# Kernel optimization log

Measured on AMD Instinct MI355X. Metric: run time of the kernel, lower is better.

## Reference

```python
import jax, jax.numpy as jnp
import numpy as np

D_MODEL = 1024
H = 16
D_K = D_MODEL // H
MASK_VALUE = -2000000000.0  # fp32 path in the original module


def setup_inputs() -> dict:
    key = jax.random.key(0)
    ks = jax.random.split(key, 7)
    B, S = 2, 2048
    scale = 1.0 / np.sqrt(D_MODEL)
    inp = {
        "q": jax.random.normal(ks[0], (B, S, D_MODEL), jnp.float32),
        "k": jax.random.normal(ks[1], (B, S, D_MODEL), jnp.float32),
        "v": jax.random.normal(ks[2], (B, S, D_MODEL), jnp.float32),
        # causal mask, broadcast over batch and heads
        "mask": jnp.tril(jnp.ones((1, 1, S, S), jnp.int32)),
        "w_q": jax.random.normal(ks[3], (D_MODEL, D_MODEL), jnp.float32) * scale,
        "w_k": jax.random.normal(ks[4], (D_MODEL, D_MODEL), jnp.float32) * scale,
        "w_v": jax.random.normal(ks[5], (D_MODEL, D_MODEL), jnp.float32) * scale,
        "w_o": jax.random.normal(ks[6], (D_MODEL, D_MODEL), jnp.float32) * scale,
    }
    return inp


def reference(q, k, v, mask, w_q, w_k, w_v, w_o):
    B, S, _ = q.shape
    # Linear(d_model, d_model, bias=False): x @ W.T  (weights stored [out, in])
    def proj(x, w):
        y = jnp.einsum('bsd,ed->bse', x, w)
        return y.reshape(B, -1, H, D_K).transpose(0, 2, 1, 3)  # [B, H, S, d_k]

    Q = proj(q, w_q)
    K = proj(k, w_k)
    V = proj(v, w_v)

    scores = jnp.einsum('bhsd,bhtd->bhst', Q, K) * (D_K ** -0.5)  # [B,H,S,S]
    scores = jnp.where(mask == 0, MASK_VALUE, scores)
    attn = jax.nn.softmax(scores, axis=-1)
    x = jnp.einsum('bhst,bhtd->bhsd', attn, V)                     # [B,H,S,d_k]
    x = x.transpose(0, 2, 1, 3).reshape(B, -1, D_MODEL)            # [B,S,d_model]
    return jnp.einsum('bsd,ed->bse', x, w_o)
```

## Files before the change

kernel.cpp:

```cpp
#include <hip/hip_runtime.h>
#include <math.h>

#define S_LEN 2048
#define DM 1024
#define NH 16
#define DK 64
#define BATCH 2
#define MS (BATCH*S_LEN)

typedef __attribute__((ext_vector_type(8))) short bf16x8;
typedef __attribute__((ext_vector_type(4))) float f32x4;
typedef __attribute__((ext_vector_type(16))) float f32x16;
typedef unsigned short u16;
typedef unsigned int u32;

__device__ __forceinline__ u16 f2b(float f) {
  union { float f; u32 u; } x; x.f = f;
  u32 r = x.u + 0x7FFFu + ((x.u >> 16) & 1u);
  return (u16)(r >> 16);
}

__device__ __forceinline__ u32 cvtpk_bf16(float lo, float hi) {
  u32 r;
  asm volatile("v_cvt_pk_bf16_f32 %0, %1, %2" : "=v"(r) : "v"(lo), "v"(hi));
  return r;
}

struct CvtArgs {
  const float* src[7];
  u16* dst[7];
  float scl[7];
  int n4[7];
};

__global__ void cvt_all(CvtArgs a) {
  const int seg = blockIdx.y;
  const float* __restrict__ in = a.src[seg];
  u16* __restrict__ out = a.dst[seg];
  const float s = a.scl[seg];
  const int n4 = a.n4[seg];
  int idx = blockIdx.x * blockDim.x + threadIdx.x;
  int stride = gridDim.x * blockDim.x;
  for (int i = idx; i < n4; i += stride) {
    float4 v = ((const float4*)in)[i];
    ushort4 o;
    o.x = f2b(v.x * s); o.y = f2b(v.y * s); o.z = f2b(v.z * s); o.w = f2b(v.w * s);
    ((ushort4*)out)[i] = o;
  }
}

__device__ __forceinline__ void gload_lds16(const u16* g, u16* l) {
  __builtin_amdgcn_global_load_lds((const __attribute__((address_space(1))) u32*)g,
                                   (__attribute__((address_space(3))) u32*)l, 16, 0, 0);
}

template<bool OUT_BF16, int BM>
__device__ __forceinline__ void gemm_body(
    const u16* __restrict__ A, const u16* __restrict__ B, void* __restrict__ Cout,
    int M, int N, int K, int bx, int by, u16* lsA, u16* lsB)
{
  constexpr int MF = BM / 32;
  const int tid = threadIdx.x;
  const int lane = tid & 63;
  const int wid = tid >> 6;
  const int wr = wid >> 1, wc = wid & 1;
  const int m0 = by * BM, n0 = bx * 128;

  f32x4 acc[MF][4];
#pragma unroll
  for (int i = 0; i < MF; ++i)
#pragma unroll
    for (int j = 0; j < 4; ++j) acc[i][j] = (f32x4){0.f, 0.f, 0.f, 0.f};

  const int ntiles = K >> 5;

#pragma unroll
  for (int i = 0; i < BM/64; ++i) {
    int u = tid + i * 256;
    gload_lds16(A + (size_t)(m0 + (u >> 2)) * K + (u & 3) * 8, &lsA[u * 8]);
  }
#pragma unroll
  for (int i = 0; i < 2; ++i) {
    int u = tid + i * 256;
    gload_lds16(B + (size_t)(n0 + (u >> 2)) * K + (u & 3) * 8, &lsB[u * 8]);
  }

  for (int kt = 0; kt < ntiles; ++kt) {
    __syncthreads();
    bf16x8 af[MF], bfr[4];
    const int kOff = (lane >> 4) * 8;
#pragma unroll
    for (int m = 0; m < MF; ++m)
      af[m] = *(const bf16x8*)&lsA[(wr * (BM/2) + m * 16 + (lane & 15)) * 32 + kOff];
#pragma unroll
    for (int n = 0; n < 4; ++n)
      bfr[n] = *(const bf16x8*)&lsB[(wc * 64 + n * 16 + (lane & 15)) * 32 + kOff];
    __syncthreads();
    if (kt + 1 < ntiles) {
      int k0 = (kt + 1) << 5;
#pragma unroll
      for (int i = 0; i < BM/64; ++i) {
        int u = tid + i * 256;
        gload_lds16(A + (size_t)(m0 + (u >> 2)) * K + k0 + (u & 3) * 8, &lsA[u * 8]);
      }
#pragma unroll
      for (int i = 0; i < 2; ++i) {
        int u = tid + i * 256;
        gload_lds16(B + (size_t)(n0 + (u >> 2)) * K + k0 + (u & 3) * 8, &lsB[u * 8]);
      }
    }
#pragma unroll
    for (int m = 0; m < MF; ++m)
#pragma unroll
      for (int n = 0; n < 4; ++n)
        acc[m][n] = __builtin_amdgcn_mfma_f32_16x16x32_bf16(af[m], bfr[n], acc[m][n], 0, 0, 0);
  }

  const int rbase = m0 + wr * (BM/2) + ((lane >> 4) << 2);
  const int cbase = n0 + wc * 64 + (lane & 15);
#pragma unroll
  for (int m = 0; m < MF; ++m)
#pragma unroll
    for (int n = 0; n < 4; ++n)
#pragma unroll
      for (int j = 0; j < 4; ++j) {
        int r = rbase + m * 16 + j;
        int c = cbase + n * 16;
        if (OUT_BF16)
          ((u16*)Cout)[(size_t)r * N + c] = f2b(acc[m][n][j]);
        else
          ((float*)Cout)[(size_t)r * N + c] = acc[m][n][j];
      }
}

struct G3Args {
  const u16* A[3];
  const u16* B[3];
  u16* C[3];
};

__global__ __launch_bounds__(256) void gemm_qkv(G3Args g) {
  __shared__ u16 lsA[128*32];
  __shared__ u16 lsB[128*32];
  const int bid = blockIdx.x;
  const int gi = bid >> 8;
  const int f = bid & 255;
  const int gx = (gi == 2) ? 32 : 8;
  const int N = (gi == 2) ? MS : DM;
  const int M = (gi == 2) ? DM : MS;
  gemm_body<true,128>(g.A[gi], g.B[gi], g.C[gi], M, N, DM,
                      f % gx, f / gx, lsA, lsB);
}

__global__ __launch_bounds__(256) void gemm_out(
    const u16* __restrict__ A, const u16* __restrict__ B, float* __restrict__ C) {
  __shared__ u16 lsA[64*32];
  __shared__ u16 lsB[128*32];
  gemm_body<false,64>(A, B, C, MS, DM, DM, blockIdx.x, blockIdx.y, lsA, lsB);
}

__global__ __launch_bounds__(256) void attn_fwd(
    const u16* __restrict__ Qp, const u16* __restrict__ Kp, const u16* __restrict__ Vt,
    u16* __restrict__ AO)
{
  __shared__ __align__(16) u16 lds_kv[4][4096];
  __shared__ float lds_l[4][2][32];
  const int tid = threadIdx.x;
  const int lane = tid & 63;
  const int w = tid >> 6;
  const int ql = lane & 31;
  const int h = lane >> 5;
  const int bid = blockIdx.x;
  const int j = 63 - (bid >> 5);
  const int bh = bid & 31;
  const int b = bh >> 4;
  const int hh = bh & 15;
  const int q0 = j * 32;
  const int qg = q0 + ql;
  const size_t baseQK = (size_t)b * S_LEN * DM + hh * DK;
  const size_t baseV  = (size_t)hh * DK * MS + (size_t)b * S_LEN;

  u16* const lk = lds_kv[w];
  u16* const lv = lds_kv[w] + 2048;

  bf16x8 qf[4];
#pragma unroll
  for (int ks = 0; ks < 4; ++ks)
    qf[ks] = *(const bf16x8*)&Qp[baseQK + (size_t)qg * DM + ks * 16 + h * 8];

  f32x16 ot[2];
#pragma unroll
  for (int n = 0; n < 2; ++n)
#pragma unroll
    for (int r = 0; r < 16; ++r) ot[n][r] = 0.f;
  float lrun = 0.f;

#define STAGE(KV0) do { \
    _Pragma("unroll") \
    for (int jj = 0; jj < 4; ++jj) { \
      int c = jj * 64 + lane; \
      int kr = c >> 3, kc = c & 7; \
      gload_lds16(Kp + baseQK + (size_t)((KV0) + kr) * DM + ((kc ^ (kr & 7)) * 8), &lk[c * 8]); \
      int vr = c >> 2, vc = c & 3; \
      gload_lds16(Vt + baseV + (size_t)vr * MS + (KV0) + ((vc ^ (vr & 3)) * 8), &lv[c * 8]); \
    } \
  } while (0)

  if (w <= j) STAGE(w * 32);

  for (int tt = w; tt <= j; tt += 4) {
    asm volatile("s_waitcnt vmcnt(0)" ::: "memory");

    bf16x8 kf[4], vf[2][2];
#pragma unroll
    for (int ks = 0; ks < 4; ++ks)
      kf[ks] = *(const bf16x8*)&lk[(ql * 8 + ((2 * ks + h) ^ (ql & 7))) * 8];
#pragma unroll
    for (int n = 0; n < 2; ++n)
#pragma unroll
      for (int kst = 0; kst < 2; ++kst)
        vf[n][kst] = *(const bf16x8*)&lv[((n * 32 + ql) * 4 + ((2 * kst + h) ^ (ql & 3))) * 8];
    asm volatile("s_waitcnt lgkmcnt(0)" ::: "memory");
    if (tt + 4 <= j) STAGE((tt + 4) * 32);

    f32x16 st;
#pragma unroll
    for (int r = 0; r < 16; ++r) st[r] = 0.f;
    __builtin_amdgcn_s_setprio(1);
#pragma unroll
    for (int ks = 0; ks < 4; ++ks)
      st = __builtin_amdgcn_mfma_f32_32x32x16_bf16(kf[ks], qf[ks], st, 0, 0, 0);
    __builtin_amdgcn_s_setprio(0);

    if (tt == j) {
#pragma unroll
      for (int r = 0; r < 16; ++r) {
        int kvg = tt * 32 + (r & 3) + 8 * (r >> 2) + 4 * h;
        if (kvg > qg) st[r] = -1e30f;
      }
    }

#pragma unroll
    for (int r = 0; r < 16; ++r) {
      float p_ = st[r];
      asm("v_exp_f32 %0, %1" : "=v"(p_) : "v"(p_));
      st[r] = p_;
    }
    {
      float t0 = st[0] + st[1], t1 = st[2] + st[3];
      float t2 = st[4] + st[5], t3 = st[6] + st[7];
      float t4 = st[8] + st[9], t5 = st[10] + st[11];
      float t6 = st[12] + st[13], t7 = st[14] + st[15];
      float u0 = t0 + t1, u1 = t2 + t3, u2 = t4 + t5, u3 = t6 + t7;
      lrun += (u0 + u1) + (u2 + u3);
    }

#pragma unroll
    for (int kst = 0; kst < 2; ++kst) {
      u32 pkg[4];
#pragma unroll
      for (int g4 = 0; g4 < 4; ++g4)
        pkg[g4] = cvtpk_bf16(st[8 * kst + 2 * g4], st[8 * kst + 2 * g4 + 1]);
      asm("v_permlane32_swap_b32 %0, %1" : "+v"(pkg[0]), "+v"(pkg[2]));
      asm("v_permlane32_swap_b32 %0, %1" : "+v"(pkg[1]), "+v"(pkg[3]));
      union { u32 u[4]; bf16x8 v; } pb;
      pb.u[0] = pkg[0]; pb.u[1] = pkg[1]; pb.u[2] = pkg[2]; pb.u[3] = pkg[3];
      __builtin_amdgcn_s_setprio(1);
#pragma unroll
      for (int n = 0; n < 2; ++n)
        ot[n] = __builtin_amdgcn_mfma_f32_32x32x16_bf16(vf[n][kst], pb.v, ot[n], 0, 0, 0);
      __builtin_amdgcn_s_setprio(0);
    }
  }

  lds_l[w][h][ql] = lrun;

  {
    float* comb = (float*)lds_kv[w];
#pragma unroll
    for (int n = 0; n < 2; ++n)
#pragma unroll
      for (int r = 0; r < 16; ++r) {
        int d = 32 * n + (r & 3) + 8 * (r >> 2) + 4 * h;
        comb[d * 32 + (ql ^ (d & 31))] = ot[n][r];
      }
  }
  __syncthreads();
  {
    const int q = tid >> 3;
    const int d0 = (tid & 7) * 8;
    float lsum = 0.f;
#pragma unroll
    for (int w2 = 0; w2 < 4; ++w2)
      lsum += lds_l[w2][0][q] + lds_l[w2][1][q];
    float inv = 1.0f / lsum;
    const float* c0 = (const float*)lds_kv[0];
    const float* c1 = (const float*)lds_kv[1];
    const float* c2 = (const float*)lds_kv[2];
    const float* c3 = (const float*)lds_kv[3];
    u32 o4[4];
#pragma unroll
    for (int ii = 0; ii < 4; ++ii) {
      int da = d0 + 2 * ii, db = da + 1;
      int ia = da * 32 + (q ^ (da & 31));
      int ib = db * 32 + (q ^ (db & 31));
      float va = c0[ia] + c1[ia] + c2[ia] + c3[ia];
      float vb = c0[ib] + c1[ib] + c2[ib] + c3[ib];
      o4[ii] = cvtpk_bf16(va * inv, vb * inv);
    }
    uint4 outv;
    outv.x = o4[0]; outv.y = o4[1]; outv.z = o4[2]; outv.w = o4[3];
    *(uint4*)&AO[baseQK + (size_t)(q0 + q) * DM + d0] = outv;
  }
#undef STAGE
}

extern "C" void kernel_launch(void* const* d_in, const int* in_sizes, int n_in,
                              void* d_out, int out_size, void* d_ws, size_t ws_size,
                              hipStream_t stream) {
  const float* q  = (const float*)d_in[0];
  const float* k  = (const float*)d_in[1];
  const float* v  = (const float*)d_in[2];
  const float* wq = (const float*)d_in[4];
  const float* wk = (const float*)d_in[5];
  const float* wv = (const float*)d_in[6];
  const float* wo = (const float*)d_in[7];

  const size_t nIn = (size_t)MS * DM;
  const size_t nW  = (size_t)DM * DM;

  u16* ws = (u16*)d_ws;
  u16* qb  = ws; ws += nIn;
  u16* kb  = ws; ws += nIn;
  u16* vb  = ws; ws += nIn;
  u16* wqb = ws; ws += nW;
  u16* wkb = ws; ws += nW;
  u16* wvb = ws; ws += nW;
  u16* wob = ws; ws += nW;
  u16* Qp  = ws; ws += nIn;
  u16* Kp  = ws; ws += nIn;
  u16* Vt  = ws; ws += nIn;
  u16* AO  = ws; ws += nIn;

  CvtArgs ca;
  const float QSCL = 0.125f * 1.44269504089f;
  ca.src[0] = q;  ca.dst[0] = qb;  ca.n4[0] = (int)(nIn / 4); ca.scl[0] = 1.f;
  ca.src[1] = k;  ca.dst[1] = kb;  ca.n4[1] = (int)(nIn / 4); ca.scl[1] = 1.f;
  ca.src[2] = v;  ca.dst[2] = vb;  ca.n4[2] = (int)(nIn / 4); ca.scl[2] = 1.f;
  ca.src[3] = wq; ca.dst[3] = wqb; ca.n4[3] = (int)(nW / 4);  ca.scl[3] = QSCL;
  ca.src[4] = wk; ca.dst[4] = wkb; ca.n4[4] = (int)(nW / 4);  ca.scl[4] = 1.f;
  ca.src[5] = wv; ca.dst[5] = wvb; ca.n4[5] = (int)(nW / 4);  ca.scl[5] = 1.f;
  ca.src[6] = wo; ca.dst[6] = wob; ca.n4[6] = (int)(nW / 4);  ca.scl[6] = 1.f;
  cvt_all<<<dim3(256, 7), 256, 0, stream>>>(ca);

  G3Args g3;
  g3.A[0] = qb;  g3.B[0] = wqb; g3.C[0] = Qp;
  g3.A[1] = kb;  g3.B[1] = wkb; g3.C[1] = Kp;
  g3.A[2] = wvb; g3.B[2] = vb;  g3.C[2] = Vt;
  gemm_qkv<<<dim3(768), 256, 0, stream>>>(g3);

  attn_fwd<<<dim3(64 * 32), 256, 0, stream>>>(Qp, Kp, Vt, AO);

  gemm_out<<<dim3(8, 64), 256, 0, stream>>>(AO, wob, (float*)d_out);
}
```

Baseline: 117.0 us.

## Double GEMM K-tile to 64 with XOR swizzle; split attention K/V staging waits

The GEMM body now stages 64-wide K tiles instead of 32, with an XOR-swizzled LDS layout that avoids bank conflicts. This halves the number of barrier pairs per tile and doubles the MFMA work between syncs, at the cost of twice the LDS per block. In attention, K and V loads are issued and waited on separately with partial vmcnt waits. The next K tile can then be fetched while the current V is still in flight, overlapping memory latency with the QK and softmax work.

```diff
diff --git a/kernel.cpp b/kernel.cpp
--- a/kernel.cpp
+++ b/kernel.cpp
@@ -72,49 +72,52 @@
 #pragma unroll
     for (int j = 0; j < 4; ++j) acc[i][j] = (f32x4){0.f, 0.f, 0.f, 0.f};
 
-  const int ntiles = K >> 5;
-
-#pragma unroll
-  for (int i = 0; i < BM/64; ++i) {
-    int u = tid + i * 256;
-    gload_lds16(A + (size_t)(m0 + (u >> 2)) * K + (u & 3) * 8, &lsA[u * 8]);
-  }
-#pragma unroll
-  for (int i = 0; i < 2; ++i) {
-    int u = tid + i * 256;
-    gload_lds16(B + (size_t)(n0 + (u >> 2)) * K + (u & 3) * 8, &lsB[u * 8]);
-  }
-
+  const int ntiles = K >> 6;
+
+#define GSTAGE(K0) do { \
+    _Pragma("unroll") \
+    for (int i = 0; i < BM/32; ++i) { \
+      int u = tid + i * 256; \
+      int row = u >> 3, c8 = u & 7; \
+      gload_lds16(A + (size_t)(m0 + row) * K + (K0) + ((c8 ^ (row & 7)) * 8), &lsA[u * 8]); \
+    } \
+    _Pragma("unroll") \
+    for (int i = 0; i < 4; ++i) { \
+      int u = tid + i * 256; \
+      int row = u >> 3, c8 = u & 7; \
+      gload_lds16(B + (size_t)(n0 + row) * K + (K0) + ((c8 ^ (row & 7)) * 8), &lsB[u * 8]); \
+    } \
+  } while (0)
+
+  GSTAGE(0);
+  const int ksel = lane >> 4;
   for (int kt = 0; kt < ntiles; ++kt) {
     __syncthreads();
-    bf16x8 af[MF], bfr[4];
-    const int kOff = (lane >> 4) * 8;
-#pragma unroll
-    for (int m = 0; m < MF; ++m)
-      af[m] = *(const bf16x8*)&lsA[(wr * (BM/2) + m * 16 + (lane & 15)) * 32 + kOff];
-#pragma unroll
-    for (int n = 0; n < 4; ++n)
-      bfr[n] = *(const bf16x8*)&lsB[(wc * 64 + n * 16 + (lane & 15)) * 32 + kOff];
+    bf16x8 af[2][MF], bfr[2][4];
+#pragma unroll
+    for (int kk = 0; kk < 2; ++kk) {
+#pragma unroll
+      for (int m = 0; m < MF; ++m) {
+        int row = wr * (BM/2) + m * 16 + (lane & 15);
+        af[kk][m] = *(const bf16x8*)&lsA[row * 64 + (((kk * 4 + ksel) ^ (row & 7)) * 8)];
+      }
+#pragma unroll
+      for (int n = 0; n < 4; ++n) {
+        int row = wc * 64 + n * 16 + (lane & 15);
+        bfr[kk][n] = *(const bf16x8*)&lsB[row * 64 + (((kk * 4 + ksel) ^ (row & 7)) * 8)];
+      }
+    }
     __syncthreads();
-    if (kt + 1 < ntiles) {
-      int k0 = (kt + 1) << 5;
-#pragma unroll
-      for (int i = 0; i < BM/64; ++i) {
-        int u = tid + i * 256;
-        gload_lds16(A + (size_t)(m0 + (u >> 2)) * K + k0 + (u & 3) * 8, &lsA[u * 8]);
-      }
-#pragma unroll
-      for (int i = 0; i < 2; ++i) {
-        int u = tid + i * 256;
-        gload_lds16(B + (size_t)(n0 + (u >> 2)) * K + k0 + (u & 3) * 8, &lsB[u * 8]);
-      }
-    }
-#pragma unroll
-    for (int m = 0; m < MF; ++m)
-#pragma unroll
-      for (int n = 0; n < 4; ++n)
-        acc[m][n] = __builtin_amdgcn_mfma_f32_16x16x32_bf16(af[m], bfr[n], acc[m][n], 0, 0, 0);
-  }
+    if (kt + 1 < ntiles) GSTAGE((kt + 1) << 6);
+#pragma unroll
+    for (int kk = 0; kk < 2; ++kk)
+#pragma unroll
+      for (int m = 0; m < MF; ++m)
+#pragma unroll
+        for (int n = 0; n < 4; ++n)
+          acc[m][n] = __builtin_amdgcn_mfma_f32_16x16x32_bf16(af[kk][m], bfr[kk][n], acc[m][n], 0, 0, 0);
+  }
+#undef GSTAGE
 
   const int rbase = m0 + wr * (BM/2) + ((lane >> 4) << 2);
   const int cbase = n0 + wc * 64 + (lane & 15);
@@ -140,8 +143,8 @@
 };
 
 __global__ __launch_bounds__(256) void gemm_qkv(G3Args g) {
-  __shared__ u16 lsA[128*32];
-  __shared__ u16 lsB[128*32];
+  __shared__ u16 lsA[128*64];
+  __shared__ u16 lsB[128*64];
   const int bid = blockIdx.x;
   const int gi = bid >> 8;
   const int f = bid & 255;
@@ -154,8 +157,8 @@
 
 __global__ __launch_bounds__(256) void gemm_out(
     const u16* __restrict__ A, const u16* __restrict__ B, float* __restrict__ C) {
-  __shared__ u16 lsA[64*32];
-  __shared__ u16 lsB[128*32];
+  __shared__ u16 lsA[64*64];
+  __shared__ u16 lsB[128*64];
   gemm_body<false,64>(A, B, C, MS, DM, DM, blockIdx.x, blockIdx.y, lsA, lsB);
 }
 
@@ -187,6 +190,7 @@
 #pragma unroll
   for (int ks = 0; ks < 4; ++ks)
     qf[ks] = *(const bf16x8*)&Qp[baseQK + (size_t)qg * DM + ks * 16 + h * 8];
+  asm volatile("s_waitcnt vmcnt(0)" ::: "memory");
 
   f32x16 ot[2];
 #pragma unroll
@@ -195,33 +199,35 @@
     for (int r = 0; r < 16; ++r) ot[n][r] = 0.f;
   float lrun = 0.f;
 
-#define STAGE(KV0) do { \
+#define STAGE_K(KV0) do { \
     _Pragma("unroll") \
     for (int jj = 0; jj < 4; ++jj) { \
       int c = jj * 64 + lane; \
       int kr = c >> 3, kc = c & 7; \
       gload_lds16(Kp + baseQK + (size_t)((KV0) + kr) * DM + ((kc ^ (kr & 7)) * 8), &lk[c * 8]); \
+    } \
+  } while (0)
+
+#define STAGE_V(KV0) do { \
+    _Pragma("unroll") \
+    for (int jj = 0; jj < 4; ++jj) { \
+      int c = jj * 64 + lane; \
       int vr = c >> 2, vc = c & 3; \
       gload_lds16(Vt + baseV + (size_t)vr * MS + (KV0) + ((vc ^ (vr & 3)) * 8), &lv[c * 8]); \
     } \
   } while (0)
 
-  if (w <= j) STAGE(w * 32);
+  if (w <= j) { STAGE_K(w * 32); STAGE_V(w * 32); }
 
   for (int tt = w; tt <= j; tt += 4) {
-    asm volatile("s_waitcnt vmcnt(0)" ::: "memory");
-
-    bf16x8 kf[4], vf[2][2];
+    const bool nx = (tt + 4 <= j);
+    asm volatile("s_waitcnt vmcnt(4)" ::: "memory");
+    bf16x8 kf[4];
 #pragma unroll
     for (int ks = 0; ks < 4; ++ks)
       kf[ks] = *(const bf16x8*)&lk[(ql * 8 + ((2 * ks + h) ^ (ql & 7))) * 8];
-#pragma unroll
-    for (int n = 0; n < 2; ++n)
-#pragma unroll
-      for (int kst = 0; kst < 2; ++kst)
-        vf[n][kst] = *(const bf16x8*)&lv[((n * 32 + ql) * 4 + ((2 * kst + h) ^ (ql & 3))) * 8];
     asm volatile("s_waitcnt lgkmcnt(0)" ::: "memory");
-    if (tt + 4 <= j) STAGE((tt + 4) * 32);
+    if (nx) STAGE_K((tt + 4) * 32);
 
     f32x16 st;
 #pragma unroll
@@ -254,6 +260,17 @@
       float u0 = t0 + t1, u1 = t2 + t3, u2 = t4 + t5, u3 = t6 + t7;
       lrun += (u0 + u1) + (u2 + u3);
     }
+
+    if (nx) { asm volatile("s_waitcnt vmcnt(4)" ::: "memory"); }
+    else    { asm volatile("s_waitcnt vmcnt(0)" ::: "memory"); }
+    bf16x8 vf[2][2];
+#pragma unroll
+    for (int n = 0; n < 2; ++n)
+#pragma unroll
+      for (int kst = 0; kst < 2; ++kst)
+        vf[n][kst] = *(const bf16x8*)&lv[((n * 32 + ql) * 4 + ((2 * kst + h) ^ (ql & 3))) * 8];
+    asm volatile("s_waitcnt lgkmcnt(0)" ::: "memory");
+    if (nx) STAGE_V((tt + 4) * 32);
 
 #pragma unroll
     for (int kst = 0; kst < 2; ++kst) {
@@ -312,7 +329,8 @@
     outv.x = o4[0]; outv.y = o4[1]; outv.z = o4[2]; outv.w = o4[3];
     *(uint4*)&AO[baseQK + (size_t)(q0 + q) * DM + d0] = outv;
   }
-#undef STAGE
+#undef STAGE_K
+#undef STAGE_V
 }
 
 extern "C" void kernel_launch(void* const* d_in, const int* in_sizes, int n_in,
```

After: 112.7 us. -3.6%, faster.

## Give each attention wave its own query tile with split K/V prefetch

Applied to the files above, without the earlier changes.

Before, the four waves of a block split the KV range of one 32-row query tile and combined partial outputs and row sums through LDS behind a block barrier. Now each wave owns its own query tile and walks the whole causal KV range alone. The grid shrinks to a quarter, and the cross-wave reduction and __syncthreads go away. K and V staging are split so the next tile's K load is issued before the softmax and V is waited on later, overlapping loads with compute. The risk is load imbalance: the waves in a block hold tiles of different lengths, so a block lasts as long as its longest wave, with less parallelism per query tile and a serial dependence on each wave's own LDS buffer.

```diff
diff --git a/kernel.cpp b/kernel.cpp
--- a/kernel.cpp
+++ b/kernel.cpp
@@ -164,15 +164,14 @@
     u16* __restrict__ AO)
 {
   __shared__ __align__(16) u16 lds_kv[4][4096];
-  __shared__ float lds_l[4][2][32];
   const int tid = threadIdx.x;
   const int lane = tid & 63;
   const int w = tid >> 6;
   const int ql = lane & 31;
   const int h = lane >> 5;
-  const int bid = blockIdx.x;
-  const int j = 63 - (bid >> 5);
-  const int bh = bid & 31;
+  const int grp = blockIdx.x >> 5;
+  const int bh = blockIdx.x & 31;
+  const int j = 63 - (grp * 4 + w);
   const int b = bh >> 4;
   const int hh = bh & 15;
   const int q0 = j * 32;
@@ -187,6 +186,7 @@
 #pragma unroll
   for (int ks = 0; ks < 4; ++ks)
     qf[ks] = *(const bf16x8*)&Qp[baseQK + (size_t)qg * DM + ks * 16 + h * 8];
+  asm volatile("s_waitcnt vmcnt(0)" ::: "memory");
 
   f32x16 ot[2];
 #pragma unroll
@@ -195,33 +195,35 @@
     for (int r = 0; r < 16; ++r) ot[n][r] = 0.f;
   float lrun = 0.f;
 
-#define STAGE(KV0) do { \
+#define STAGE_K(KV0) do { \
     _Pragma("unroll") \
     for (int jj = 0; jj < 4; ++jj) { \
       int c = jj * 64 + lane; \
       int kr = c >> 3, kc = c & 7; \
       gload_lds16(Kp + baseQK + (size_t)((KV0) + kr) * DM + ((kc ^ (kr & 7)) * 8), &lk[c * 8]); \
+    } \
+  } while (0)
+
+#define STAGE_V(KV0) do { \
+    _Pragma("unroll") \
+    for (int jj = 0; jj < 4; ++jj) { \
+      int c = jj * 64 + lane; \
       int vr = c >> 2, vc = c & 3; \
       gload_lds16(Vt + baseV + (size_t)vr * MS + (KV0) + ((vc ^ (vr & 3)) * 8), &lv[c * 8]); \
     } \
   } while (0)
 
-  if (w <= j) STAGE(w * 32);
-
-  for (int tt = w; tt <= j; tt += 4) {
-    asm volatile("s_waitcnt vmcnt(0)" ::: "memory");
-
-    bf16x8 kf[4], vf[2][2];
+  STAGE_K(0); STAGE_V(0);
+
+  for (int tt = 0; tt <= j; ++tt) {
+    const bool nx = (tt < j);
+    asm volatile("s_waitcnt vmcnt(4)" ::: "memory");
+    bf16x8 kf[4];
 #pragma unroll
     for (int ks = 0; ks < 4; ++ks)
       kf[ks] = *(const bf16x8*)&lk[(ql * 8 + ((2 * ks + h) ^ (ql & 7))) * 8];
-#pragma unroll
-    for (int n = 0; n < 2; ++n)
-#pragma unroll
-      for (int kst = 0; kst < 2; ++kst)
-        vf[n][kst] = *(const bf16x8*)&lv[((n * 32 + ql) * 4 + ((2 * kst + h) ^ (ql & 3))) * 8];
     asm volatile("s_waitcnt lgkmcnt(0)" ::: "memory");
-    if (tt + 4 <= j) STAGE((tt + 4) * 32);
+    if (nx) STAGE_K((tt + 1) * 32);
 
     f32x16 st;
 #pragma unroll
@@ -255,6 +257,17 @@
       lrun += (u0 + u1) + (u2 + u3);
     }
 
+    if (nx) { asm volatile("s_waitcnt vmcnt(4)" ::: "memory"); }
+    else    { asm volatile("s_waitcnt vmcnt(0)" ::: "memory"); }
+    bf16x8 vf[2][2];
+#pragma unroll
+    for (int n = 0; n < 2; ++n)
+#pragma unroll
+      for (int kst = 0; kst < 2; ++kst)
+        vf[n][kst] = *(const bf16x8*)&lv[((n * 32 + ql) * 4 + ((2 * kst + h) ^ (ql & 3))) * 8];
+    asm volatile("s_waitcnt lgkmcnt(0)" ::: "memory");
+    if (nx) STAGE_V((tt + 1) * 32);
+
 #pragma unroll
     for (int kst = 0; kst < 2; ++kst) {
       u32 pkg[4];
@@ -273,8 +286,8 @@
     }
   }
 
-  lds_l[w][h][ql] = lrun;
-
+  lrun += __int_as_float(__shfl_xor(__float_as_int(lrun), 32, 64));
+  const float inv = 1.0f / lrun;
   {
     float* comb = (float*)lds_kv[w];
 #pragma unroll
@@ -282,37 +295,30 @@
 #pragma unroll
       for (int r = 0; r < 16; ++r) {
         int d = 32 * n + (r & 3) + 8 * (r >> 2) + 4 * h;
-        comb[d * 32 + (ql ^ (d & 31))] = ot[n][r];
-      }
-  }
-  __syncthreads();
+        comb[d * 32 + (ql ^ (d & 31))] = ot[n][r] * inv;
+      }
+  }
   {
-    const int q = tid >> 3;
-    const int d0 = (tid & 7) * 8;
-    float lsum = 0.f;
-#pragma unroll
-    for (int w2 = 0; w2 < 4; ++w2)
-      lsum += lds_l[w2][0][q] + lds_l[w2][1][q];
-    float inv = 1.0f / lsum;
-    const float* c0 = (const float*)lds_kv[0];
-    const float* c1 = (const float*)lds_kv[1];
-    const float* c2 = (const float*)lds_kv[2];
-    const float* c3 = (const float*)lds_kv[3];
-    u32 o4[4];
-#pragma unroll
-    for (int ii = 0; ii < 4; ++ii) {
-      int da = d0 + 2 * ii, db = da + 1;
-      int ia = da * 32 + (q ^ (da & 31));
-      int ib = db * 32 + (q ^ (db & 31));
-      float va = c0[ia] + c1[ia] + c2[ia] + c3[ia];
-      float vb = c0[ib] + c1[ib] + c2[ib] + c3[ib];
-      o4[ii] = cvtpk_bf16(va * inv, vb * inv);
-    }
-    uint4 outv;
-    outv.x = o4[0]; outv.y = o4[1]; outv.z = o4[2]; outv.w = o4[3];
-    *(uint4*)&AO[baseQK + (size_t)(q0 + q) * DM + d0] = outv;
-  }
-#undef STAGE
+    const float* combr = (const float*)lds_kv[w];
+    const int q = lane >> 1;
+    const int dbase = (lane & 1) * 32;
+#pragma unroll
+    for (int i = 0; i < 4; ++i) {
+      u32 o4[4];
+#pragma unroll
+      for (int e = 0; e < 4; ++e) {
+        int da = dbase + i * 8 + 2 * e, db = da + 1;
+        float va = combr[da * 32 + (q ^ (da & 31))];
+        float vb = combr[db * 32 + (q ^ (db & 31))];
+        o4[e] = cvtpk_bf16(va, vb);
+      }
+      uint4 outv;
+      outv.x = o4[0]; outv.y = o4[1]; outv.z = o4[2]; outv.w = o4[3];
+      *(uint4*)&AO[baseQK + (size_t)(q0 + q) * DM + dbase + i * 8] = outv;
+    }
+  }
+#undef STAGE_K
+#undef STAGE_V
 }
 
 extern "C" void kernel_launch(void* const* d_in, const int* in_sizes, int n_in,
@@ -359,7 +365,7 @@
   g3.A[2] = wvb; g3.B[2] = vb;  g3.C[2] = Vt;
   gemm_qkv<<<dim3(768), 256, 0, stream>>>(g3);
 
-  attn_fwd<<<dim3(64 * 32), 256, 0, stream>>>(Qp, Kp, Vt, AO);
+  attn_fwd<<<dim3(16 * 32), 256, 0, stream>>>(Qp, Kp, Vt, AO);
 
   gemm_out<<<dim3(8, 64), 256, 0, stream>>>(AO, wob, (float*)d_out);
 }
```

After: 128.7 us. +10.1%, slower.

## Split K and V tile staging to overlap V loads with QK compute

Applied to the files above, without the earlier changes.

Splits the per-tile global-to-LDS staging into separate K and V phases. The kernel now waits only for K (vmcnt(4)) before the QK MFMA and waits for V just before the PV MFMA. The prefetch of the next V tile is issued after the current V fragments have been read. Staging addresses are precomputed once as per-lane pointers and advanced each step, which removes repeated address arithmetic. The finer-grained waits depend on the in-flight load count exactly matching 4, which makes the code fragile to reordering.

```diff
diff --git a/kernel.cpp b/kernel.cpp
--- a/kernel.cpp
+++ b/kernel.cpp
@@ -187,6 +187,7 @@
 #pragma unroll
   for (int ks = 0; ks < 4; ++ks)
     qf[ks] = *(const bf16x8*)&Qp[baseQK + (size_t)qg * DM + ks * 16 + h * 8];
+  asm volatile("s_waitcnt vmcnt(0)" ::: "memory");
 
   f32x16 ot[2];
 #pragma unroll
@@ -195,33 +196,46 @@
     for (int r = 0; r < 16; ++r) ot[n][r] = 0.f;
   float lrun = 0.f;
 
-#define STAGE(KV0) do { \
+  const u16* kptr[4];
+  const u16* vptr[4];
+#pragma unroll
+  for (int jj = 0; jj < 4; ++jj) {
+    int c = jj * 64 + lane;
+    int kr = c >> 3, kc = c & 7;
+    kptr[jj] = Kp + baseQK + (size_t)(w * 32 + kr) * DM + (kc ^ (kr & 7)) * 8;
+    int vr = c >> 2, vc = c & 3;
+    vptr[jj] = Vt + baseV + (size_t)vr * MS + w * 32 + (vc ^ (vr & 3)) * 8;
+  }
+
+#define STAGE_K() do { \
     _Pragma("unroll") \
     for (int jj = 0; jj < 4; ++jj) { \
       int c = jj * 64 + lane; \
-      int kr = c >> 3, kc = c & 7; \
-      gload_lds16(Kp + baseQK + (size_t)((KV0) + kr) * DM + ((kc ^ (kr & 7)) * 8), &lk[c * 8]); \
-      int vr = c >> 2, vc = c & 3; \
-      gload_lds16(Vt + baseV + (size_t)vr * MS + (KV0) + ((vc ^ (vr & 3)) * 8), &lv[c * 8]); \
+      gload_lds16(kptr[jj], &lk[c * 8]); \
+      kptr[jj] += (size_t)128 * DM; \
     } \
   } while (0)
 
-  if (w <= j) STAGE(w * 32);
+#define STAGE_V() do { \
+    _Pragma("unroll") \
+    for (int jj = 0; jj < 4; ++jj) { \
+      int c = jj * 64 + lane; \
+      gload_lds16(vptr[jj], &lv[c * 8]); \
+      vptr[jj] += 128; \
+    } \
+  } while (0)
+
+  if (w <= j) { STAGE_K(); STAGE_V(); }
 
   for (int tt = w; tt <= j; tt += 4) {
-    asm volatile("s_waitcnt vmcnt(0)" ::: "memory");
-
-    bf16x8 kf[4], vf[2][2];
+    const bool nx = (tt + 4 <= j);
+    asm volatile("s_waitcnt vmcnt(4)" ::: "memory");
+    bf16x8 kf[4];
 #pragma unroll
     for (int ks = 0; ks < 4; ++ks)
       kf[ks] = *(const bf16x8*)&lk[(ql * 8 + ((2 * ks + h) ^ (ql & 7))) * 8];
-#pragma unroll
-    for (int n = 0; n < 2; ++n)
-#pragma unroll
-      for (int kst = 0; kst < 2; ++kst)
-        vf[n][kst] = *(const bf16x8*)&lv[((n * 32 + ql) * 4 + ((2 * kst + h) ^ (ql & 3))) * 8];
     asm volatile("s_waitcnt lgkmcnt(0)" ::: "memory");
-    if (tt + 4 <= j) STAGE((tt + 4) * 32);
+    if (nx) STAGE_K();
 
     f32x16 st;
 #pragma unroll
@@ -254,6 +268,17 @@
       float u0 = t0 + t1, u1 = t2 + t3, u2 = t4 + t5, u3 = t6 + t7;
       lrun += (u0 + u1) + (u2 + u3);
     }
+
+    if (nx) { asm volatile("s_waitcnt vmcnt(4)" ::: "memory"); }
+    else    { asm volatile("s_waitcnt vmcnt(0)" ::: "memory"); }
+    bf16x8 vf[2][2];
+#pragma unroll
+    for (int n = 0; n < 2; ++n)
+#pragma unroll
+      for (int kst = 0; kst < 2; ++kst)
+        vf[n][kst] = *(const bf16x8*)&lv[((n * 32 + ql) * 4 + ((2 * kst + h) ^ (ql & 3))) * 8];
+    asm volatile("s_waitcnt lgkmcnt(0)" ::: "memory");
+    if (nx) STAGE_V();
 
 #pragma unroll
     for (int kst = 0; kst < 2; ++kst) {
@@ -312,7 +337,8 @@
     outv.x = o4[0]; outv.y = o4[1]; outv.z = o4[2]; outv.w = o4[3];
     *(uint4*)&AO[baseQK + (size_t)(q0 + q) * DM + d0] = outv;
   }
-#undef STAGE
+#undef STAGE_K
+#undef STAGE_V
 }
 
 extern "C" void kernel_launch(void* const* d_in, const int* in_sizes, int n_in,
```

New measurement: 117.1 us. No clear change (+0.1%).
